# Optimization experiments

Hardware: AMD Instinct MI355X
Metric: run time of the kernel (lower is better)

## Reference

```python
import jax, jax.numpy as jnp
import numpy as np

N = 10000
E = 160000
D_IN = 128
H = 1024
NUM_GRAPHS = 8
EPS = 1e-5


def setup_inputs() -> dict:
    key = jax.random.key(0)
    ks = jax.random.split(key, 24)
    x = jax.random.normal(ks[0], (N, D_IN), dtype=jnp.float32)
    edge_index = jax.random.randint(ks[1], (2, E), 0, N, dtype=jnp.int32)
    batch = jnp.sort(jax.random.randint(ks[2], (N,), 0, NUM_GRAPHS, dtype=jnp.int32))
    s = 0.02
    W1 = jax.random.normal(ks[3], (D_IN, H), dtype=jnp.float32) * s
    b1 = jnp.zeros((H,), jnp.float32)
    Wh = jax.random.normal(ks[4], (3, H, H), dtype=jnp.float32) * s
    bh = jnp.zeros((3, H), jnp.float32)
    ln_g = jnp.ones((4, H), jnp.float32)
    ln_b = jnp.zeros((4, H), jnp.float32)
    vW = jax.random.normal(ks[5], (6, H, H), dtype=jnp.float32) * s
    vb = jnp.zeros((6, H), jnp.float32)
    vWo = jax.random.normal(ks[6], (H, 1), dtype=jnp.float32) * s
    vbo = jnp.zeros((1,), jnp.float32)
    return {"x": x, "edge_index": edge_index, "batch": batch,
            "W1": W1, "b1": b1, "Wh": Wh, "bh": bh,
            "ln_g": ln_g, "ln_b": ln_b, "vW": vW, "vb": vb,
            "vWo": vWo, "vbo": vbo}


def _layer_norm(x, g, b):
    m = jnp.mean(x, axis=-1, keepdims=True)
    v = jnp.mean(jnp.square(x - m), axis=-1, keepdims=True)
    return (x - m) * jax.lax.rsqrt(v + EPS) * g + b


def reference(x, edge_index, batch, W1, b1, Wh, bh, ln_g, ln_b, vW, vb, vWo, vbo):
    # GCNConv: add self loops, symmetric normalization, x @ W, scatter-add at dst, + bias
    loops = jnp.arange(N, dtype=edge_index.dtype)
    src = jnp.concatenate([edge_index[0], loops])
    dst = jnp.concatenate([edge_index[1], loops])
    deg = jax.ops.segment_sum(jnp.ones_like(dst, dtype=x.dtype), dst, num_segments=N)
    dinv = jax.lax.rsqrt(jnp.maximum(deg, 1.0))
    norm = (dinv[src] * dinv[dst])[:, None]  # [E+N, 1]

    def gcn(h, W, b):
        h = h @ W                              # [N, H]
        msg = h[src] * norm                    # gather + scale [E+N, H]
        return jax.ops.segment_sum(msg, dst, num_segments=N) + b

    x1 = gcn(x, W1, b1)
    h = jax.nn.relu(_layer_norm(x1, ln_g[0], ln_b[0]))
    x2 = gcn(h, Wh[0], bh[0])
    h = jax.nn.relu(_layer_norm(x2 + x1, ln_g[1], ln_b[1]))
    x3 = gcn(h, Wh[1], bh[1])
    h = jax.nn.relu(_layer_norm(x3 + x1, ln_g[2], ln_b[2]))
    x4 = gcn(h, Wh[2], bh[2])
    node_embeddings = jax.nn.relu(_layer_norm(x4 + h, ln_g[3], ln_b[3]))

    # global mean pool per graph
    counts = jax.ops.segment_sum(jnp.ones((N,), x.dtype), batch, num_segments=NUM_GRAPHS)
    sums = jax.ops.segment_sum(node_embeddings, batch, num_segments=NUM_GRAPHS)
    graph_embedding = sums / jnp.maximum(counts, 1.0)[:, None]

    v = graph_embedding
    for i in range(6):
        v = jax.nn.relu(v @ vW[i] + vb[i])
    state_value = (v @ vWo + vbo).squeeze(-1)
    return node_embeddings, graph_embedding, state_value
```

## Files before the change

### kernel.cpp

```cpp
#include <hip/hip_runtime.h>
#include <stdint.h>

#define N_NODES 10000
#define E_EDGES 160000
#define DIN 128
#define H 1024
#define NUM_GRAPHS 8
#define LN_EPS 1e-5f

typedef unsigned short u16;
typedef __attribute__((ext_vector_type(8))) short short8;
typedef __attribute__((ext_vector_type(8))) unsigned short ushort8v;
typedef __attribute__((ext_vector_type(4))) float f32x4;

__device__ __forceinline__ float bf2f(u16 v) { return __uint_as_float(((unsigned)v) << 16); }
__device__ __forceinline__ u16 f2bf(float f) {
    unsigned u = __float_as_uint(f);
    u += 0x7fffu + ((u >> 16) & 1u);
    return (u16)(u >> 16);
}

__global__ void k_init(int* cnt, int* goff, float* __restrict__ gsum,
                       float* __restrict__ vbuf, const float* __restrict__ vb) {
    int i = blockIdx.x * 256 + threadIdx.x;
    if (i < N_NODES) cnt[i] = 0;
    if (i <= NUM_GRAPHS) goff[i] = 0;
    if (i < NUM_GRAPHS * H) gsum[i] = 0.f;
    if (i < 6 * H) {
        int il = i >> 10, j = i & (H - 1);
        float b = vb[il * H + j];
        float* base = vbuf + (size_t)(il + 1) * NUM_GRAPHS * H;
#pragma unroll
        for (int g = 0; g < NUM_GRAPHS; g++) base[g * H + j] = b;
    }
}

__global__ void k_count(const int* __restrict__ dst, int* __restrict__ cnt) {
    int e = blockIdx.x * 256 + threadIdx.x;
    if (e < E_EDGES) atomicAdd(&cnt[dst[e]], 1);
}

__global__ __launch_bounds__(1024) void k_scan(const int* __restrict__ cnt, int* __restrict__ offs,
                                               int* __restrict__ cursor, float* __restrict__ dinv) {
    __shared__ int wsum[16];
    __shared__ int carry_s;
    int tid = threadIdx.x;
    int lane = tid & 63, wv = tid >> 6;
    if (tid == 0) carry_s = 0;
    __syncthreads();
    for (int base = 0; base < N_NODES; base += 1024) {
        int i = base + tid;
        int v = (i < N_NODES) ? cnt[i] : 0;
        int x = v;
#pragma unroll
        for (int off = 1; off < 64; off <<= 1) {
            int t = __shfl_up(x, off);
            if (lane >= off) x += t;
        }
        if (lane == 63) wsum[wv] = x;
        __syncthreads();
        int carry = carry_s;
        if (wv == 0) {
            int ws = (lane < 16) ? wsum[lane] : 0;
#pragma unroll
            for (int off = 1; off < 16; off <<= 1) {
                int t = __shfl_up(ws, off);
                if (lane >= off) ws += t;
            }
            if (lane < 16) wsum[lane] = ws;
        }
        __syncthreads();
        int wbase = (wv > 0) ? wsum[wv - 1] : 0;
        int incl = wbase + x;
        int excl = incl - v;
        if (i < N_NODES) {
            offs[i] = carry + excl;
            cursor[i] = carry + excl;
            dinv[i] = rsqrtf((float)(v + 1));
        }
        if (tid == 1023) carry_s = carry + incl;
        __syncthreads();
    }
    if (tid == 0) offs[N_NODES] = carry_s;
}

__global__ void k_fill(const int* __restrict__ src, const int* __restrict__ dst,
                       int* __restrict__ cursor, int* __restrict__ csr_src) {
    int e = blockIdx.x * 256 + threadIdx.x;
    if (e < E_EDGES) {
        int d = dst[e];
        int slot = atomicAdd(&cursor[d], 1);
        csr_src[slot] = src[e];
    }
}

__global__ void k_gbound(const int* __restrict__ batch, int* __restrict__ goff) {
    int i = blockIdx.x * 256 + threadIdx.x;
    if (i >= N_NODES) return;
    int b0 = batch[i];
    int b1 = (i + 1 < N_NODES) ? batch[i + 1] : NUM_GRAPHS;
    for (int g = b0 + 1; g <= b1; g++) goff[g] = i + 1;
}

__global__ void k_cvt(const float* __restrict__ src, u16* __restrict__ dst, int n) {
    int i = blockIdx.x * 256 + threadIdx.x;
    if (i < n) dst[i] = f2bf(src[i]);
}

__global__ void k_transpose_cvt(const float* __restrict__ src, u16* __restrict__ dst, int R, int C) {
    __shared__ float tile[32][33];
    int tx = threadIdx.x, ty = threadIdx.y;
    int x = blockIdx.x * 32 + tx;
#pragma unroll
    for (int i = 0; i < 32; i += 8) {
        int y = blockIdx.y * 32 + ty + i;
        tile[ty + i][tx] = (y < R && x < C) ? src[(size_t)y * C + x] : 0.f;
    }
    __syncthreads();
    int xo = blockIdx.y * 32 + tx;
#pragma unroll
    for (int i = 0; i < 32; i += 8) {
        int yo = blockIdx.x * 32 + ty + i;
        if (yo < C && xo < R) dst[(size_t)yo * R + xo] = f2bf(tile[tx][ty + i]);
    }
}

__global__ __launch_bounds__(64) void k_agg_x(const u16* __restrict__ xb, const float* __restrict__ dinv,
                                              const int* __restrict__ offs, const int* __restrict__ csr_src,
                                              u16* __restrict__ xa) {
    __shared__ float s_dv[64];
    __shared__ int s_id[64];
    int d = blockIdx.x;
    int tid = threadIdx.x;
    int c = tid * 2;
    float dd = dinv[d];
    float a0, a1;
    {
        unsigned v = *(const unsigned*)(xb + (size_t)d * DIN + c);
        a0 = dd * bf2f((u16)(v & 0xffffu));
        a1 = dd * bf2f((u16)(v >> 16));
    }
    int beg = offs[d], end = offs[d + 1];
    for (int chunk = beg; chunk < end; chunk += 64) {
        int nthis = end - chunk;
        if (nthis > 64) nthis = 64;
        int np = (nthis + 7) & ~7;
        __syncthreads();
        if (tid < nthis) {
            int s = csr_src[chunk + tid];
            s_id[tid] = s;
            s_dv[tid] = dinv[s];
        } else if (tid < np) {
            s_id[tid] = d;
            s_dv[tid] = 0.f;
        }
        __syncthreads();
        for (int i = 0; i < np; i += 8) {
            unsigned v[8];
            float e[8];
#pragma unroll
            for (int u = 0; u < 8; u++) {
                int s = s_id[i + u];
                e[u] = s_dv[i + u];
                v[u] = *(const unsigned*)(xb + (size_t)s * DIN + c);
            }
#pragma unroll
            for (int u = 0; u < 8; u++) {
                a0 += e[u] * bf2f((u16)(v[u] & 0xffffu));
                a1 += e[u] * bf2f((u16)(v[u] >> 16));
            }
        }
    }
    a0 *= dd;
    a1 *= dd;
    unsigned o = ((unsigned)f2bf(a1) << 16) | (unsigned)f2bf(a0);
    *(unsigned*)(xa + (size_t)d * DIN + c) = o;
}

__global__ __launch_bounds__(256) void k_agg_col(const u16* __restrict__ t, const float* __restrict__ dinv,
                                                 const int* __restrict__ offs, const int* __restrict__ csr_src,
                                                 u16* __restrict__ abuf) {
    int chunk = blockIdx.x & 7;
    int grp = threadIdx.x >> 4;
    int ln = threadIdx.x & 15;
    int d = (blockIdx.x >> 3) * 16 + grp;
    size_t col = (size_t)chunk * 128 + (size_t)ln * 8;
    const u16* tc = t + col;
    float dd = dinv[d];
    float a[8];
    {
        ushort8v v = *(const ushort8v*)(tc + (size_t)d * H);
#pragma unroll
        for (int i = 0; i < 8; i++) a[i] = dd * bf2f(v[i]);
    }
    int e = offs[d], end = offs[d + 1];
    for (; e + 2 <= end; e += 2) {
        int s0 = csr_src[e], s1 = csr_src[e + 1];
        float w0 = dinv[s0], w1 = dinv[s1];
        ushort8v v0 = *(const ushort8v*)(tc + (size_t)s0 * H);
        ushort8v v1 = *(const ushort8v*)(tc + (size_t)s1 * H);
#pragma unroll
        for (int j = 0; j < 8; j++) a[j] += w0 * bf2f(v0[j]) + w1 * bf2f(v1[j]);
    }
    if (e < end) {
        int s0 = csr_src[e];
        float w0 = dinv[s0];
        ushort8v v0 = *(const ushort8v*)(tc + (size_t)s0 * H);
#pragma unroll
        for (int j = 0; j < 8; j++) a[j] += w0 * bf2f(v0[j]);
    }
    ushort8v o;
#pragma unroll
    for (int i = 0; i < 8; i++) o[i] = f2bf(dd * a[i]);
    __builtin_nontemporal_store(o, (ushort8v*)(abuf + (size_t)d * H + col));
}

template <int MODE>
__global__ __launch_bounds__(128) void k_ln(const u16* __restrict__ a, const u16* __restrict__ resid,
                                            const float* __restrict__ bias, const float* __restrict__ gamma,
                                            const float* __restrict__ beta,
                                            u16* __restrict__ out_bf, u16* __restrict__ out_pre,
                                            float* __restrict__ out_f32) {
    __shared__ float red1[2], red2[2];
    int d = blockIdx.x;
    int tid = threadIdx.x;
    int c = tid * 8;
    float x[8];
    {
        ushort8v v = *(const ushort8v*)(a + (size_t)d * H + c);
#pragma unroll
        for (int i = 0; i < 8; i++) x[i] = bf2f(v[i]) + bias[c + i];
    }
    if (MODE >= 1) {
        ushort8v r = *(const ushort8v*)(resid + (size_t)d * H + c);
#pragma unroll
        for (int i = 0; i < 8; i++) x[i] += bf2f(r[i]);
    }
    if (MODE == 0) {
        ushort8v p;
#pragma unroll
        for (int i = 0; i < 8; i++) p[i] = f2bf(x[i]);
        *(ushort8v*)(out_pre + (size_t)d * H + c) = p;
    }
    float s1 = 0.f, s2 = 0.f;
#pragma unroll
    for (int i = 0; i < 8; i++) { s1 += x[i]; s2 += x[i] * x[i]; }
#pragma unroll
    for (int off = 32; off > 0; off >>= 1) {
        s1 += __shfl_down(s1, off);
        s2 += __shfl_down(s2, off);
    }
    int lane = tid & 63, wv = tid >> 6;
    if (lane == 0) { red1[wv] = s1; red2[wv] = s2; }
    __syncthreads();
    float sum = red1[0] + red1[1];
    float ssq = red2[0] + red2[1];
    float mean = sum * (1.f / H);
    float var = fmaxf(ssq * (1.f / H) - mean * mean, 0.f);
    float inv = rsqrtf(var + LN_EPS);
    float y[8];
#pragma unroll
    for (int i = 0; i < 8; i++)
        y[i] = fmaxf((x[i] - mean) * inv * gamma[c + i] + beta[c + i], 0.f);
    if (MODE == 2) {
        float4 o0 = {y[0], y[1], y[2], y[3]};
        float4 o1 = {y[4], y[5], y[6], y[7]};
        *(float4*)(out_f32 + (size_t)d * H + c) = o0;
        *(float4*)(out_f32 + (size_t)d * H + c + 4) = o1;
    } else {
        ushort8v o;
#pragma unroll
        for (int i = 0; i < 8; i++) o[i] = f2bf(y[i]);
        *(ushort8v*)(out_bf + (size_t)d * H + c) = o;
    }
}

typedef __attribute__((address_space(1))) const unsigned int gas_u32;
typedef __attribute__((address_space(3))) unsigned int las_u32;
__device__ __forceinline__ void gld_lds16(const void* g, void* l) {
    __builtin_amdgcn_global_load_lds((gas_u32*)g, (las_u32*)l, 16, 0, 0);
}

__global__ __launch_bounds__(256) void k_gemm(const u16* __restrict__ A, const u16* __restrict__ B,
                                              u16* __restrict__ C, int M, int Nn, int K) {
    __shared__ __align__(16) u16 sA[128 * 32];
    __shared__ __align__(16) u16 sB[128 * 32];
    int tid = threadIdx.x;
    int lane = tid & 63;
    int w = tid >> 6;
    int wm = w >> 1, wn = w & 1;
    int m0 = blockIdx.x * 128;
    int n0 = blockIdx.y * 128;

    f32x4 zero = {0.f, 0.f, 0.f, 0.f};
    f32x4 acc[4][4];
#pragma unroll
    for (int i = 0; i < 4; i++)
#pragma unroll
        for (int j = 0; j < 4; j++) acc[i][j] = zero;

    int srow = w * 32 + (lane >> 2);
    int scol = (lane & 3) * 8;
    u16* laA = sA + w * 1024;
    u16* laB = sB + w * 1024;

    for (int k0 = 0; k0 < K; k0 += 32) {
        __syncthreads();
#pragma unroll
        for (int q = 0; q < 2; q++) {
            int rA = m0 + srow + q * 16;
            rA = rA < M ? rA : M - 1;
            gld_lds16(A + (size_t)rA * K + k0 + scol, laA + q * 512);
            gld_lds16(B + (size_t)(n0 + srow + q * 16) * K + k0 + scol, laB + q * 512);
        }
        __syncthreads();

        short8 af[4], bv[4];
#pragma unroll
        for (int mi = 0; mi < 4; mi++)
            af[mi] = *(const short8*)(sA + (wm * 64 + mi * 16 + (lane & 15)) * 32 + (lane >> 4) * 8);
#pragma unroll
        for (int ni = 0; ni < 4; ni++)
            bv[ni] = *(const short8*)(sB + (wn * 64 + ni * 16 + (lane & 15)) * 32 + (lane >> 4) * 8);
#pragma unroll
        for (int mi = 0; mi < 4; mi++)
#pragma unroll
            for (int ni = 0; ni < 4; ni++)
                acc[mi][ni] = __builtin_amdgcn_mfma_f32_16x16x32_bf16(af[mi], bv[ni], acc[mi][ni], 0, 0, 0);
    }

    int rbase = m0 + wm * 64 + (lane >> 4) * 4;
    int cbase = n0 + wn * 64 + (lane & 15);
#pragma unroll
    for (int mi = 0; mi < 4; mi++) {
#pragma unroll
        for (int r = 0; r < 4; r++) {
            int row = rbase + mi * 16 + r;
            if (row < M) {
#pragma unroll
                for (int ni = 0; ni < 4; ni++)
                    C[(size_t)row * Nn + cbase + ni * 16] = f2bf(acc[mi][ni][r]);
            }
        }
    }
}

#define PC_NODES 16
__global__ __launch_bounds__(256) void k_pool_acc(const float* __restrict__ ne, const int* __restrict__ batch,
                                                  float* __restrict__ gsum) {
    int c = blockIdx.x * 256 + threadIdx.x;
    int nbeg = blockIdx.y * PC_NODES;
    int nend = nbeg + PC_NODES;
    if (nend > N_NODES) nend = N_NODES;
    float acc = 0.f;
    int curg = batch[nbeg];
    for (int n = nbeg; n < nend; n++) {
        int g = batch[n];
        if (g != curg) {
            atomicAdd(&gsum[curg * H + c], acc);
            acc = 0.f;
            curg = g;
        }
        acc += ne[(size_t)n * H + c];
    }
    atomicAdd(&gsum[curg * H + c], acc);
}

__global__ __launch_bounds__(256) void k_pool_fin(const float* __restrict__ gsum, const int* __restrict__ goff,
                                                  float* __restrict__ v0, float* __restrict__ ge_out) {
    int g = blockIdx.y;
    int c = blockIdx.x * 256 + threadIdx.x;
    float cntf = (float)(goff[g + 1] - goff[g]);
    float m = gsum[g * H + c] / fmaxf(cntf, 1.f);
    v0[g * H + c] = m;
    ge_out[(size_t)g * H + c] = m;
}

template <bool RELU_IN>
__global__ __launch_bounds__(256) void k_mlp_acc(const float* __restrict__ vin, const float* __restrict__ W,
                                                 float* __restrict__ vout) {
    __shared__ float sk[64];
    int g = blockIdx.y;
    int j = blockIdx.x * 256 + threadIdx.x;
    int k0 = blockIdx.z * 64;
    if (threadIdx.x < 64) {
        float v = vin[g * H + k0 + threadIdx.x];
        sk[threadIdx.x] = RELU_IN ? fmaxf(v, 0.f) : v;
    }
    __syncthreads();
    float acc = 0.f;
#pragma unroll
    for (int k = 0; k < 64; k++) acc += sk[k] * W[(size_t)(k0 + k) * H + j];
    atomicAdd(&vout[g * H + j], acc);
}

__global__ void k_head(const float* __restrict__ vin, const float* __restrict__ Wo,
                       const float* __restrict__ bo, float* __restrict__ out) {
    int g = blockIdx.x;
    int tid = threadIdx.x;
    float s = 0.f;
    for (int k = tid; k < H; k += 256) s += fmaxf(vin[g * H + k], 0.f) * Wo[k];
#pragma unroll
    for (int off = 32; off > 0; off >>= 1) s += __shfl_down(s, off);
    __shared__ float p[4];
    if ((tid & 63) == 0) p[tid >> 6] = s;
    __syncthreads();
    if (tid == 0) out[g] = p[0] + p[1] + p[2] + p[3] + bo[0];
}

extern "C" void kernel_launch(void* const* d_in, const int* in_sizes, int n_in,
                              void* d_out, int out_size, void* d_ws, size_t ws_size,
                              hipStream_t stream) {
    const float* x = (const float*)d_in[0];
    const int* ei = (const int*)d_in[1];
    const int* batch = (const int*)d_in[2];
    const float* W1 = (const float*)d_in[3];
    const float* b1 = (const float*)d_in[4];
    const float* Wh = (const float*)d_in[5];
    const float* bh = (const float*)d_in[6];
    const float* ln_g = (const float*)d_in[7];
    const float* ln_b = (const float*)d_in[8];
    const float* vW = (const float*)d_in[9];
    const float* vb = (const float*)d_in[10];
    const float* vWo = (const float*)d_in[11];
    const float* vbo = (const float*)d_in[12];
    const int* esrc = ei;
    const int* edst = ei + E_EDGES;

    char* ws = (char*)d_ws;
    size_t off = 0;
    auto carve = [&](size_t bytes) -> char* {
        char* p = ws + off;
        off += (bytes + 255) & ~(size_t)255;
        return p;
    };
    float* dinv = (float*)carve(N_NODES * 4);
    int* cnt = (int*)carve(N_NODES * 4);
    int* offs = (int*)carve((N_NODES + 1) * 4);
    int* cursor = (int*)carve(N_NODES * 4);
    int* csr_src = (int*)carve(E_EDGES * 4);
    int* goff = (int*)carve((NUM_GRAPHS + 1) * 4);
    float* gsum = (float*)carve(NUM_GRAPHS * H * 4);
    float* vbuf = (float*)carve((size_t)7 * NUM_GRAPHS * H * 4);
    u16* xb = (u16*)carve((size_t)N_NODES * DIN * 2);
    u16* xa = (u16*)carve((size_t)N_NODES * DIN * 2);
    u16* Wt = (u16*)carve((size_t)H * H * 2);
    u16* tbuf = (u16*)carve((size_t)N_NODES * H * 2);
    u16* hbuf = (u16*)carve((size_t)N_NODES * H * 2);
    u16* x1buf = (u16*)carve((size_t)N_NODES * H * 2);
    u16* abuf = (u16*)carve((size_t)N_NODES * H * 2);

    float* out_ne = (float*)d_out;
    float* out_ge = out_ne + (size_t)N_NODES * H;
    float* out_sv = out_ge + (size_t)NUM_GRAPHS * H;

    k_init<<<(N_NODES + 255) / 256, 256, 0, stream>>>(cnt, goff, gsum, vbuf, vb);
    k_count<<<(E_EDGES + 255) / 256, 256, 0, stream>>>(edst, cnt);
    k_scan<<<1, 1024, 0, stream>>>(cnt, offs, cursor, dinv);
    k_fill<<<(E_EDGES + 255) / 256, 256, 0, stream>>>(esrc, edst, cursor, csr_src);
    k_gbound<<<(N_NODES + 255) / 256, 256, 0, stream>>>(batch, goff);
    k_cvt<<<(N_NODES * DIN + 255) / 256, 256, 0, stream>>>(x, xb, N_NODES * DIN);

    dim3 tb(32, 8);
    dim3 gg((N_NODES + 127) / 128, H / 128);
    int agg_grid = (N_NODES / 16) * 8;

    k_agg_x<<<N_NODES, 64, 0, stream>>>(xb, dinv, offs, csr_src, xa);
    k_transpose_cvt<<<dim3(H / 32, DIN / 32), tb, 0, stream>>>(W1, Wt, DIN, H);
    k_gemm<<<gg, 256, 0, stream>>>(xa, Wt, tbuf, N_NODES, H, DIN);
    k_ln<0><<<N_NODES, 128, 0, stream>>>(tbuf, nullptr, b1, ln_g, ln_b, hbuf, x1buf, nullptr);

    k_transpose_cvt<<<dim3(H / 32, H / 32), tb, 0, stream>>>(Wh + 0 * (size_t)H * H, Wt, H, H);
    k_gemm<<<gg, 256, 0, stream>>>(hbuf, Wt, tbuf, N_NODES, H, H);
    k_agg_col<<<agg_grid, 256, 0, stream>>>(tbuf, dinv, offs, csr_src, abuf);
    k_ln<1><<<N_NODES, 128, 0, stream>>>(abuf, x1buf, bh, ln_g + H, ln_b + H, hbuf, nullptr, nullptr);

    k_transpose_cvt<<<dim3(H / 32, H / 32), tb, 0, stream>>>(Wh + 1 * (size_t)H * H, Wt, H, H);
    k_gemm<<<gg, 256, 0, stream>>>(hbuf, Wt, tbuf, N_NODES, H, H);
    k_agg_col<<<agg_grid, 256, 0, stream>>>(tbuf, dinv, offs, csr_src, abuf);
    k_ln<1><<<N_NODES, 128, 0, stream>>>(abuf, x1buf, bh + H, ln_g + 2 * H, ln_b + 2 * H, hbuf, nullptr, nullptr);

    k_transpose_cvt<<<dim3(H / 32, H / 32), tb, 0, stream>>>(Wh + 2 * (size_t)H * H, Wt, H, H);
    k_gemm<<<gg, 256, 0, stream>>>(hbuf, Wt, tbuf, N_NODES, H, H);
    k_agg_col<<<agg_grid, 256, 0, stream>>>(tbuf, dinv, offs, csr_src, abuf);
    k_ln<2><<<N_NODES, 128, 0, stream>>>(abuf, hbuf, bh + 2 * H, ln_g + 3 * H, ln_b + 3 * H, nullptr, nullptr, out_ne);

    k_pool_acc<<<dim3(H / 256, (N_NODES + PC_NODES - 1) / PC_NODES), 256, 0, stream>>>(out_ne, batch, gsum);
    k_pool_fin<<<dim3(H / 256, NUM_GRAPHS), 256, 0, stream>>>(gsum, goff, vbuf, out_ge);

    dim3 mg(H / 256, NUM_GRAPHS, 16);
    k_mlp_acc<false><<<mg, 256, 0, stream>>>(vbuf, vW, vbuf + (size_t)1 * NUM_GRAPHS * H);
    for (int i = 1; i < 6; i++)
        k_mlp_acc<true><<<mg, 256, 0, stream>>>(vbuf + (size_t)i * NUM_GRAPHS * H, vW + (size_t)i * H * H,
                                                vbuf + (size_t)(i + 1) * NUM_GRAPHS * H);
    k_head<<<NUM_GRAPHS, 256, 0, stream>>>(vbuf + (size_t)6 * NUM_GRAPHS * H, vWo, vbo, out_sv);
}
```

Measured before the change: 496.5 us.

## Double-buffer GEMM LDS with swizzle, remap blocks, batch weight transposes, unroll aggregation

The GEMM now double-buffers its LDS tiles, issuing the next k-slice's global-to-LDS loads before running the MFMAs on the current slice. It also XOR-swizzles LDS columns to cut bank conflicts and remaps the 1D grid so blocks that share B tiles run together for L2 reuse. The three hidden-layer weight transposes become a single batched launch into a separate buffer, which removes two launches and the reuse of one shared Wt buffer. The column aggregation loop is unrolled to four edges per iteration so more gathers are in flight. The costs are double the LDS per block and higher register pressure in the aggregation kernel.

```diff
diff --git a/kernel.cpp b/kernel.cpp
--- a/kernel.cpp
+++ b/kernel.cpp
@@ -107,8 +107,10 @@
     if (i < n) dst[i] = f2bf(src[i]);
 }
 
-__global__ void k_transpose_cvt(const float* __restrict__ src, u16* __restrict__ dst, int R, int C) {
+__global__ void k_transpose_cvt(const float* __restrict__ src0, u16* __restrict__ dst0, int R, int C) {
     __shared__ float tile[32][33];
+    const float* src = src0 + (size_t)blockIdx.z * R * C;
+    u16* dst = dst0 + (size_t)blockIdx.z * R * C;
     int tx = threadIdx.x, ty = threadIdx.y;
     int x = blockIdx.x * 32 + tx;
 #pragma unroll
@@ -194,15 +196,18 @@
         for (int i = 0; i < 8; i++) a[i] = dd * bf2f(v[i]);
     }
     int e = offs[d], end = offs[d + 1];
-    for (; e + 2 <= end; e += 2) {
-        int s0 = csr_src[e], s1 = csr_src[e + 1];
-        float w0 = dinv[s0], w1 = dinv[s1];
+    for (; e + 4 <= end; e += 4) {
+        int s0 = csr_src[e], s1 = csr_src[e + 1], s2 = csr_src[e + 2], s3 = csr_src[e + 3];
+        float w0 = dinv[s0], w1 = dinv[s1], w2 = dinv[s2], w3 = dinv[s3];
         ushort8v v0 = *(const ushort8v*)(tc + (size_t)s0 * H);
         ushort8v v1 = *(const ushort8v*)(tc + (size_t)s1 * H);
-#pragma unroll
-        for (int j = 0; j < 8; j++) a[j] += w0 * bf2f(v0[j]) + w1 * bf2f(v1[j]);
-    }
-    if (e < end) {
+        ushort8v v2 = *(const ushort8v*)(tc + (size_t)s2 * H);
+        ushort8v v3 = *(const ushort8v*)(tc + (size_t)s3 * H);
+#pragma unroll
+        for (int j = 0; j < 8; j++)
+            a[j] += w0 * bf2f(v0[j]) + w1 * bf2f(v1[j]) + w2 * bf2f(v2[j]) + w3 * bf2f(v3[j]);
+    }
+    for (; e < end; e++) {
         int s0 = csr_src[e];
         float w0 = dinv[s0];
         ushort8v v0 = *(const ushort8v*)(tc + (size_t)s0 * H);
@@ -283,14 +288,22 @@
 
 __global__ __launch_bounds__(256) void k_gemm(const u16* __restrict__ A, const u16* __restrict__ B,
                                               u16* __restrict__ C, int M, int Nn, int K) {
-    __shared__ __align__(16) u16 sA[128 * 32];
-    __shared__ __align__(16) u16 sB[128 * 32];
+    __shared__ __align__(16) u16 sA[2][128 * 32];
+    __shared__ __align__(16) u16 sB[2][128 * 32];
+    int mtiles = (M + 127) >> 7;
+    int L = blockIdx.x;
+    int cls = L & 7;
+    int s = L >> 3;
+    int nt = s & 7;
+    int mt = (s >> 3) * 8 + cls;
+    if (mt >= mtiles) return;
+    int m0 = mt << 7;
+    int n0 = nt << 7;
+
     int tid = threadIdx.x;
     int lane = tid & 63;
     int w = tid >> 6;
     int wm = w >> 1, wn = w & 1;
-    int m0 = blockIdx.x * 128;
-    int n0 = blockIdx.y * 128;
 
     f32x4 zero = {0.f, 0.f, 0.f, 0.f};
     f32x4 acc[4][4];
@@ -300,33 +313,44 @@
         for (int j = 0; j < 4; j++) acc[i][j] = zero;
 
     int srow = w * 32 + (lane >> 2);
-    int scol = (lane & 3) * 8;
-    u16* laA = sA + w * 1024;
-    u16* laB = sB + w * 1024;
-
-    for (int k0 = 0; k0 < K; k0 += 32) {
-        __syncthreads();
+    int scol = (((lane & 3) ^ ((lane >> 3) & 3))) * 8;
+
+    auto STAGE = [&](int p, int k0) {
 #pragma unroll
         for (int q = 0; q < 2; q++) {
             int rA = m0 + srow + q * 16;
             rA = rA < M ? rA : M - 1;
-            gld_lds16(A + (size_t)rA * K + k0 + scol, laA + q * 512);
-            gld_lds16(B + (size_t)(n0 + srow + q * 16) * K + k0 + scol, laB + q * 512);
-        }
-        __syncthreads();
+            gld_lds16(A + (size_t)rA * K + k0 + scol, sA[p] + w * 1024 + q * 512);
+            gld_lds16(B + (size_t)(n0 + srow + q * 16) * K + k0 + scol, sB[p] + w * 1024 + q * 512);
+        }
+    };
+
+    int NK = K >> 5;
+    STAGE(0, 0);
+    __syncthreads();
+
+    int rchunk = ((lane >> 4) ^ ((lane >> 1) & 3)) * 8;
+    int arow = (wm * 64 + (lane & 15)) * 32 + rchunk;
+    int brow = (wn * 64 + (lane & 15)) * 32 + rchunk;
+
+    for (int kt = 0; kt < NK; kt++) {
+        int cur = kt & 1;
+        if (kt + 1 < NK) STAGE(cur ^ 1, (kt + 1) << 5);
 
         short8 af[4], bv[4];
 #pragma unroll
         for (int mi = 0; mi < 4; mi++)
-            af[mi] = *(const short8*)(sA + (wm * 64 + mi * 16 + (lane & 15)) * 32 + (lane >> 4) * 8);
+            af[mi] = *(const short8*)(sA[cur] + arow + mi * 16 * 32);
 #pragma unroll
         for (int ni = 0; ni < 4; ni++)
-            bv[ni] = *(const short8*)(sB + (wn * 64 + ni * 16 + (lane & 15)) * 32 + (lane >> 4) * 8);
+            bv[ni] = *(const short8*)(sB[cur] + brow + ni * 16 * 32);
 #pragma unroll
         for (int mi = 0; mi < 4; mi++)
 #pragma unroll
             for (int ni = 0; ni < 4; ni++)
                 acc[mi][ni] = __builtin_amdgcn_mfma_f32_16x16x32_bf16(af[mi], bv[ni], acc[mi][ni], 0, 0, 0);
+
+        __syncthreads();
     }
 
     int rbase = m0 + wm * 64 + (lane >> 4) * 4;
@@ -444,7 +468,8 @@
     float* vbuf = (float*)carve((size_t)7 * NUM_GRAPHS * H * 4);
     u16* xb = (u16*)carve((size_t)N_NODES * DIN * 2);
     u16* xa = (u16*)carve((size_t)N_NODES * DIN * 2);
-    u16* Wt = (u16*)carve((size_t)H * H * 2);
+    u16* Wt1 = (u16*)carve((size_t)H * DIN * 2);
+    u16* Wt3 = (u16*)carve((size_t)3 * H * H * 2);
     u16* tbuf = (u16*)carve((size_t)N_NODES * H * 2);
     u16* hbuf = (u16*)carve((size_t)N_NODES * H * 2);
     u16* x1buf = (u16*)carve((size_t)N_NODES * H * 2);
@@ -462,26 +487,26 @@
     k_cvt<<<(N_NODES * DIN + 255) / 256, 256, 0, stream>>>(x, xb, N_NODES * DIN);
 
     dim3 tb(32, 8);
-    dim3 gg((N_NODES + 127) / 128, H / 128);
+    int mtiles = (N_NODES + 127) / 128;
+    int gemm_grid = 8 * 8 * ((mtiles + 7) / 8);
     int agg_grid = (N_NODES / 16) * 8;
 
+    k_transpose_cvt<<<dim3(H / 32, DIN / 32, 1), tb, 0, stream>>>(W1, Wt1, DIN, H);
+    k_transpose_cvt<<<dim3(H / 32, H / 32, 3), tb, 0, stream>>>(Wh, Wt3, H, H);
+
     k_agg_x<<<N_NODES, 64, 0, stream>>>(xb, dinv, offs, csr_src, xa);
-    k_transpose_cvt<<<dim3(H / 32, DIN / 32), tb, 0, stream>>>(W1, Wt, DIN, H);
-    k_gemm<<<gg, 256, 0, stream>>>(xa, Wt, tbuf, N_NODES, H, DIN);
+    k_gemm<<<gemm_grid, 256, 0, stream>>>(xa, Wt1, tbuf, N_NODES, H, DIN);
     k_ln<0><<<N_NODES, 128, 0, stream>>>(tbuf, nullptr, b1, ln_g, ln_b, hbuf, x1buf, nullptr);
 
-    k_transpose_cvt<<<dim3(H / 32, H / 32), tb, 0, stream>>>(Wh + 0 * (size_t)H * H, Wt, H, H);
-    k_gemm<<<gg, 256, 0, stream>>>(hbuf, Wt, tbuf, N_NODES, H, H);
+    k_gemm<<<gemm_grid, 256, 0, stream>>>(hbuf, Wt3, tbuf, N_NODES, H, H);
     k_agg_col<<<agg_grid, 256, 0, stream>>>(tbuf, dinv, offs, csr_src, abuf);
     k_ln<1><<<N_NODES, 128, 0, stream>>>(abuf, x1buf, bh, ln_g + H, ln_b + H, hbuf, nullptr, nullptr);
 
-    k_transpose_cvt<<<dim3(H / 32, H / 32), tb, 0, stream>>>(Wh + 1 * (size_t)H * H, Wt, H, H);
-    k_gemm<<<gg, 256, 0, stream>>>(hbuf, Wt, tbuf, N_NODES, H, H);
+    k_gemm<<<gemm_grid, 256, 0, stream>>>(hbuf, Wt3 + (size_t)H * H, tbuf, N_NODES, H, H);
     k_agg_col<<<agg_grid, 256, 0, stream>>>(tbuf, dinv, offs, csr_src, abuf);
     k_ln<1><<<N_NODES, 128, 0, stream>>>(abuf, x1buf, bh + H, ln_g + 2 * H, ln_b + 2 * H, hbuf, nullptr, nullptr);
 
-    k_transpose_cvt<<<dim3(H / 32, H / 32), tb, 0, stream>>>(Wh + 2 * (size_t)H * H, Wt, H, H);
-    k_gemm<<<gg, 256, 0, stream>>>(hbuf, Wt, tbuf, N_NODES, H, H);
+    k_gemm<<<gemm_grid, 256, 0, stream>>>(hbuf, Wt3 + (size_t)2 * H * H, tbuf, N_NODES, H, H);
     k_agg_col<<<agg_grid, 256, 0, stream>>>(tbuf, dinv, offs, csr_src, abuf);
     k_ln<2><<<N_NODES, 128, 0, stream>>>(abuf, hbuf, bh + 2 * H, ln_g + 3 * H, ln_b + 3 * H, nullptr, nullptr, out_ne);
 
```

New measurement: 445.7 us. -10.2%, faster.
